# Optimization experiments

Measured on AMD Instinct MI355X. Metric: run time of the kernel, lower is better.

Reference implementation:

```python
import jax, jax.numpy as jnp
import numpy as np

B, N, C, HEADS = 4, 8192, 512, 8


def setup_inputs() -> dict:
    key = jax.random.key(0)
    k1, k2, k3, k4, k5 = jax.random.split(key, 5)
    s = 1.0 / np.sqrt(C)
    return {
        "x": jax.random.normal(k1, (B, N, C), dtype=jnp.float32),
        "w_qkv": jax.random.normal(k2, (3 * C, C), dtype=jnp.float32) * s,
        "b_qkv": jax.random.normal(k3, (3 * C,), dtype=jnp.float32) * 0.01,
        "w_fc": jax.random.normal(k4, (C, C), dtype=jnp.float32) * s,
        "b_fc": jax.random.normal(k5, (C,), dtype=jnp.float32) * 0.01,
        "heads": HEADS,
    }


def reference(x, w_qkv, b_qkv, w_fc, b_fc, heads):
    b, n, c = x.shape
    d = c // heads
    scale = d ** (-0.5)
    # torch Linear: y = x @ W.T + b
    qkv = (x @ w_qkv.T + b_qkv).reshape(b, n, 3, heads, d)
    q, k, v = qkv[:, :, 0], qkv[:, :, 1], qkv[:, :, 2]  # [b,n,h,d]
    # NOTE: source does NOT move heads to dim 1, so attention is over the
    # heads axis: dots is [b, n, h, h].
    dots = jnp.einsum("bnhd,bngd->bnhg", q, k) * scale
    dots = jnp.clip(dots, -50.0, 50.0)
    attn = jax.nn.softmax(dots, axis=-1)
    out = jnp.einsum("bnhg,bngd->bnhd", attn, v)  # [b,n,h,d]
    # transpose(1,2).reshape(B,N,C) exactly as in torch (scrambles n/h)
    out = out.transpose(0, 2, 1, 3).reshape(b, n, c)
    return out @ w_fc.T + b_fc
```

## Files before the change

### kernel.cpp

```cpp
#include <hip/hip_runtime.h>
#include <hip/hip_bf16.h>
#include <stdint.h>


typedef __bf16 bf16x8 __attribute__((ext_vector_type(8)));
typedef float f32x4 __attribute__((ext_vector_type(4)));

__device__ __forceinline__ unsigned short f2bf(float f) {
  unsigned u = __float_as_uint(f);
  u += 0x7fffu + ((u >> 16) & 1u);
  return (unsigned short)(u >> 16);
}
__device__ __forceinline__ unsigned pk2(float a, float b) {
  return (unsigned)f2bf(a) | ((unsigned)f2bf(b) << 16);
}
__device__ __forceinline__ void unpk2(unsigned u, float& a, float& b) {
  a = __uint_as_float(u << 16);
  b = __uint_as_float(u & 0xffff0000u);
}
__device__ __forceinline__ void gload_lds16(const void* g, void* l) {
  __builtin_amdgcn_global_load_lds((const __attribute__((address_space(1))) void*)g,
                                   (__attribute__((address_space(3))) void*)l,
                                   16, 0, 0);
}

__global__ __launch_bounds__(256) void cvt_all(const float* __restrict__ x,
                                               const float* __restrict__ wq,
                                               const float* __restrict__ wf,
                                               unsigned short* __restrict__ xb,
                                               unsigned short* __restrict__ wqb,
                                               unsigned short* __restrict__ wfb) {
  const int n0 = 2097152;
  const int n1 = 98304;
  int i = blockIdx.x * 256 + threadIdx.x;
  const float* in;
  unsigned short* ob;
  int j;
  if (i < n0) {
    in = x; ob = xb; j = i;
  } else if (i < n0 + n1) {
    in = wq; ob = wqb; j = i - n0;
  } else {
    in = wf; ob = wfb; j = i - n0 - n1;
  }
  const float4* p = (const float4*)in;
  float4 a = p[j * 2];
  float4 b = p[j * 2 + 1];
  uint4 o;
  o.x = pk2(a.x, a.y);
  o.y = pk2(a.z, a.w);
  o.z = pk2(b.x, b.y);
  o.w = pk2(b.z, b.w);
  ((uint4*)ob)[j] = o;
}


#define STG(S, BUF)                                                                       \
  do {                                                                                    \
    int _k0 = (S) * 32;                                                                   \
    gload_lds16(Ag + (size_t)(bm0 + srowA0) * KDIM + _k0 + skofA0,                        \
                lds + (BUF) * 24576 + dstA0);                                             \
    gload_lds16(Ag + (size_t)(bm0 + srowA1) * KDIM + _k0 + skofA1,                        \
                lds + (BUF) * 24576 + dstA1);                                             \
    gload_lds16(Bg + (size_t)(bn0 + srowB) * KDIM + _k0 + skofB,                          \
                lds + (BUF) * 24576 + 16384 + dstB);                                      \
  } while (0)

#define STEP(S, BC, BN)                                                                   \
  do {                                                                                    \
    const int s_ = (S);                                                                   \
    asm volatile("s_waitcnt vmcnt(0)" ::: "memory");             \
    __builtin_amdgcn_s_barrier();                                \
    __builtin_amdgcn_sched_barrier(0);                                                    \
    if (s_ + 2 < NKT) STG(s_ + 2, (s_ + 2) % 3);                                          \
    const char* nab = lds + ((s_ + 1) % 3) * 24576 + wm * 4096 + pbase;                   \
    const char* nbb = lds + ((s_ + 1) % 3) * 24576 + 16384 + wn * 4096 + pbase;           \
    if (s_ + 1 < NKT) {                                                                   \
      BN[0] = *(const bf16x8*)(nbb);                                                      \
      BN[1] = *(const bf16x8*)(nbb + 1024);                                               \
      BN[2] = *(const bf16x8*)(nbb + 2048);                                               \
      BN[3] = *(const bf16x8*)(nbb + 3072);                                               \
    }                                                                                     \
    __builtin_amdgcn_s_setprio(1);                                                        \
    _Pragma("unroll") for (int _i = 0; _i < 4; ++_i) {                                    \
      acc[_i][0] = __builtin_amdgcn_mfma_f32_16x16x32_bf16(af[_i], BC[0], acc[_i][0], 0, 0, 0); \
      acc[_i][1] = __builtin_amdgcn_mfma_f32_16x16x32_bf16(af[_i], BC[1], acc[_i][1], 0, 0, 0); \
      acc[_i][2] = __builtin_amdgcn_mfma_f32_16x16x32_bf16(af[_i], BC[2], acc[_i][2], 0, 0, 0); \
      acc[_i][3] = __builtin_amdgcn_mfma_f32_16x16x32_bf16(af[_i], BC[3], acc[_i][3], 0, 0, 0); \
      if (s_ + 1 < NKT) af[_i] = *(const bf16x8*)(nab + _i * 1024);                       \
    }                                                                                     \
    __builtin_amdgcn_s_setprio(0);                                                        \
  } while (0)

template <bool OUT_BF16, int KDIM>
__global__ __launch_bounds__(512, 4) void gemmp(const __hip_bfloat16* __restrict__ Ag,
                                                const __hip_bfloat16* __restrict__ Bg,
                                                const float* __restrict__ bias,
                                                void* __restrict__ C,
                                                int M, int N, int NT) {
  __shared__ __align__(16) char lds[73728];

  const int tid = threadIdx.x;
  const int wv = tid >> 6;
  const int ln = tid & 63;
  const int lrow = ln & 15;
  const int kg = ln >> 4;
  const int wm = wv >> 1;
  const int wn = wv & 1;

  int nwg = gridDim.x;
  int cpx = nwg >> 3;
  int bs = (blockIdx.x & 7) * cpx + (blockIdx.x >> 3);
  const int bm0 = (bs / NT) * 256;
  const int bn0 = (bs % NT) * 128;

  const int pbase = (lrow >> 1) * 128 + ((((lrow & 1) << 2) | kg) ^ ((lrow >> 1) & 7)) * 16;

  int srowA0, skofA0, dstA0, srowA1, skofA1, dstA1, srowB, skofB, dstB;
  {
    int L0 = wv * 1024 + ln * 16;
    int rp0 = L0 >> 7, T0 = ((L0 >> 4) & 7) ^ (rp0 & 7);
    srowA0 = rp0 * 2 + (T0 >> 2);
    skofA0 = (T0 & 3) * 8;
    dstA0 = wv * 1024;
    int L1 = 8192 + L0;
    int rp1 = L1 >> 7, T1 = ((L1 >> 4) & 7) ^ (rp1 & 7);
    srowA1 = rp1 * 2 + (T1 >> 2);
    skofA1 = (T1 & 3) * 8;
    dstA1 = 8192 + wv * 1024;
    srowB = srowA0;
    skofB = skofA0;
    dstB = wv * 1024;
  }

  f32x4 acc[4][4] = {};
  bf16x8 af[4], bs0[4], bs1[4];

  constexpr int NKT = KDIM >> 5;

  STG(0, 0);
  STG(1, 1);
  asm volatile("s_waitcnt vmcnt(3)" ::: "memory");
  __builtin_amdgcn_s_barrier();
  __builtin_amdgcn_sched_barrier(0);
  {
    const char* ab0 = lds + wm * 4096 + pbase;
    const char* bb0 = lds + 16384 + wn * 4096 + pbase;
#pragma unroll
    for (int i = 0; i < 4; ++i) af[i] = *(const bf16x8*)(ab0 + i * 1024);
#pragma unroll
    for (int j = 0; j < 4; ++j) bs0[j] = *(const bf16x8*)(bb0 + j * 1024);
  }

#pragma unroll
  for (int sp = 0; sp < NKT / 2; ++sp) {
    STEP(2 * sp, bs0, bs1);
    STEP(2 * sp + 1, bs1, bs0);
  }
  __syncthreads();

  if (OUT_BF16) {
    unsigned short* tile = (unsigned short*)lds;
#pragma unroll
    for (int fi = 0; fi < 4; ++fi) {
#pragma unroll
      for (int cj = 0; cj < 4; ++cj) {
        int col = wn * 64 + cj * 16 + lrow;
        float bv = bias[bn0 + col];
#pragma unroll
        for (int r = 0; r < 4; ++r) {
          int row = wm * 64 + fi * 16 + kg * 4 + r;
          int sc = (((col >> 3) ^ (row & 7)) << 3) | (col & 7);
          tile[row * 128 + sc] = f2bf(acc[fi][cj][r] + bv);
        }
      }
    }
    __syncthreads();
#pragma unroll
    for (int it = 0; it < 8; ++it) {
      int id = it * 512 + tid;
      int row = id >> 4;
      int c = id & 15;
      uint4 v = *(const uint4*)(lds + row * 256 + ((c ^ (row & 7)) << 4));
      *(uint4*)((unsigned short*)C + (size_t)(bm0 + row) * N + bn0 + c * 8) = v;
    }
  } else {
    float* tilef = (float*)lds;
#pragma unroll
    for (int pass = 0; pass < 2; ++pass) {
      if ((wm >> 1) == pass) {
#pragma unroll
        for (int fi = 0; fi < 4; ++fi) {
#pragma unroll
          for (int cj = 0; cj < 4; ++cj) {
            int col = wn * 64 + cj * 16 + lrow;
            float bv = bias[bn0 + col];
#pragma unroll
            for (int r = 0; r < 4; ++r) {
              int row = (wm & 1) * 64 + fi * 16 + kg * 4 + r;
              int sc = (((col >> 2) ^ (row & 7)) << 2) | (col & 3);
              tilef[row * 128 + sc] = acc[fi][cj][r] + bv;
            }
          }
        }
      }
      __syncthreads();
#pragma unroll
      for (int it = 0; it < 8; ++it) {
        int id = it * 512 + tid;
        int row = id >> 5;
        int c = id & 31;
        uint4 v = *(const uint4*)(lds + row * 512 + ((c ^ (row & 7)) << 4));
        *(uint4*)((float*)C + (size_t)(bm0 + pass * 128 + row) * N + bn0 + c * 4) = v;
      }
      __syncthreads();
    }
  }
}

__global__ __launch_bounds__(256) void attn_tok(const __hip_bfloat16* __restrict__ qkv,
                                                __hip_bfloat16* __restrict__ outp,
                                                int ntok, int npb) {
  const int wv = threadIdx.x >> 6;
  const int ln = threadIdx.x & 63;
  const int t = blockIdx.x * 4 + wv;
  if (t >= ntok) return;
  const int m = ln & 7;

  const __hip_bfloat16* row = qkv + (size_t)t * 1536;
  uint4 qr = *(const uint4*)(row + ln * 8);
  uint4 kr = *(const uint4*)(row + 512 + ln * 8);
  uint4 vr = *(const uint4*)(row + 1024 + ln * 8);

  float qf[8];
  unpk2(qr.x, qf[0], qf[1]);
  unpk2(qr.y, qf[2], qf[3]);
  unpk2(qr.z, qf[4], qf[5]);
  unpk2(qr.w, qf[6], qf[7]);
  unsigned kw[4] = {kr.x, kr.y, kr.z, kr.w};
  unsigned vw[4] = {vr.x, vr.y, vr.z, vr.w};

  float dt[8];
#pragma unroll
  for (int g = 0; g < 8; ++g) {
    int src = g * 8 + m;
    float s = 0.f;
#pragma unroll
    for (int j4 = 0; j4 < 4; ++j4) {
      unsigned kk = __shfl(kw[j4], src, 64);
      float a, b;
      unpk2(kk, a, b);
      s += qf[j4 * 2] * a + qf[j4 * 2 + 1] * b;
    }
    s += __shfl_xor(s, 1, 64);
    s += __shfl_xor(s, 2, 64);
    s += __shfl_xor(s, 4, 64);
    dt[g] = s;
  }

  float mx = -1e30f;
#pragma unroll
  for (int g = 0; g < 8; ++g) {
    dt[g] = fminf(fmaxf(dt[g] * 0.125f, -50.f), 50.f);
    mx = fmaxf(mx, dt[g]);
  }
  float p[8], ssum = 0.f;
#pragma unroll
  for (int g = 0; g < 8; ++g) {
    p[g] = __expf(dt[g] - mx);
    ssum += p[g];
  }
  float inv = 1.f / ssum;

  float o[8] = {0, 0, 0, 0, 0, 0, 0, 0};
#pragma unroll
  for (int g = 0; g < 8; ++g) {
    int src = g * 8 + m;
    float ag = p[g] * inv;
#pragma unroll
    for (int j4 = 0; j4 < 4; ++j4) {
      unsigned vv = __shfl(vw[j4], src, 64);
      float a, b;
      unpk2(vv, a, b);
      o[j4 * 2] += ag * a;
      o[j4 * 2 + 1] += ag * b;
    }
  }

  const int h = ln >> 3;
  const int b = t / npb, n = t % npb;
  size_t dst = (size_t)b * npb * 512 + (size_t)(h * (npb >> 3) + (n >> 3)) * 512 +
               (size_t)((n & 7) * 64 + m * 8);
  uint4 ov;
  ov.x = pk2(o[0], o[1]);
  ov.y = pk2(o[2], o[3]);
  ov.z = pk2(o[4], o[5]);
  ov.w = pk2(o[6], o[7]);
  *(uint4*)(outp + dst) = ov;
}

extern "C" void kernel_launch(void* const* d_in, const int* in_sizes, int n_in,
                              void* d_out, int out_size, void* d_ws, size_t ws_size,
                              hipStream_t stream) {
  const float* x = (const float*)d_in[0];
  const float* w_qkv = (const float*)d_in[1];
  const float* b_qkv = (const float*)d_in[2];
  const float* w_fc = (const float*)d_in[3];
  const float* b_fc = (const float*)d_in[4];
  float* out = (float*)d_out;

  const int M = 32768;
  const int Cc = 512, N3 = 1536;

  __hip_bfloat16* xb = (__hip_bfloat16*)d_ws;
  __hip_bfloat16* wqkvb = xb + (size_t)M * Cc;
  __hip_bfloat16* wfcb = wqkvb + (size_t)N3 * Cc;
  __hip_bfloat16* qkvb = wfcb + (size_t)Cc * Cc;
  __hip_bfloat16* attb = qkvb + (size_t)M * N3;

  cvt_all<<<8704, 256, 0, stream>>>(x, w_qkv, w_fc, (unsigned short*)xb,
                                    (unsigned short*)wqkvb, (unsigned short*)wfcb);

  gemmp<true, 512><<<(M / 256) * (N3 / 128), 512, 0, stream>>>(xb, wqkvb, b_qkv, qkvb, M, N3,
                                                               N3 / 128);
  attn_tok<<<M / 4, 256, 0, stream>>>(qkvb, attb, M, 8192);
  gemmp<false, 512><<<(M / 256) * (Cc / 128), 512, 0, stream>>>(attb, wfcb, b_fc, out, M, Cc,
                                                                Cc / 128);
}
```

Measured before the change: 146.3 us.

## Fuse fp32-to-bf16 conversion of x into the QKV GEMM A-tile loader

```diff
diff --git a/kernel.cpp b/kernel.cpp
--- a/kernel.cpp
+++ b/kernel.cpp
@@ -24,24 +24,19 @@
                                    16, 0, 0);
 }
 
-__global__ __launch_bounds__(256) void cvt_all(const float* __restrict__ x,
-                                               const float* __restrict__ wq,
-                                               const float* __restrict__ wf,
-                                               unsigned short* __restrict__ xb,
-                                               unsigned short* __restrict__ wqb,
-                                               unsigned short* __restrict__ wfb) {
-  const int n0 = 2097152;
+__global__ __launch_bounds__(256) void cvt_w(const float* __restrict__ wq,
+                                             const float* __restrict__ wf,
+                                             unsigned short* __restrict__ wqb,
+                                             unsigned short* __restrict__ wfb) {
   const int n1 = 98304;
   int i = blockIdx.x * 256 + threadIdx.x;
   const float* in;
   unsigned short* ob;
   int j;
-  if (i < n0) {
-    in = x; ob = xb; j = i;
-  } else if (i < n0 + n1) {
-    in = wq; ob = wqb; j = i - n0;
+  if (i < n1) {
+    in = wq; ob = wqb; j = i;
   } else {
-    in = wf; ob = wfb; j = i - n0 - n1;
+    in = wf; ob = wfb; j = i - n1;
   }
   const float4* p = (const float4*)in;
   float4 a = p[j * 2];
@@ -55,24 +50,54 @@
 }
 
 
-#define STG(S, BUF)                                                                       \
+#define STG_A_DMA(S, BUF)                                                                 \
   do {                                                                                    \
     int _k0 = (S) * 32;                                                                   \
-    gload_lds16(Ag + (size_t)(bm0 + srowA0) * KDIM + _k0 + skofA0,                        \
+    gload_lds16(Ab + (size_t)(bm0 + srowA0) * KDIM + _k0 + skofA0,                        \
                 lds + (BUF) * 24576 + dstA0);                                             \
-    gload_lds16(Ag + (size_t)(bm0 + srowA1) * KDIM + _k0 + skofA1,                        \
+    gload_lds16(Ab + (size_t)(bm0 + srowA1) * KDIM + _k0 + skofA1,                        \
                 lds + (BUF) * 24576 + dstA1);                                             \
-    gload_lds16(Bg + (size_t)(bn0 + srowB) * KDIM + _k0 + skofB,                          \
-                lds + (BUF) * 24576 + 16384 + dstB);                                      \
+  } while (0)
+
+#define STG_B(S, BUF)                                                                     \
+  gload_lds16(Bg + (size_t)(bn0 + srowB) * KDIM + (S) * 32 + skofB,                       \
+              lds + (BUF) * 24576 + 16384 + dstB)
+
+#define ISSUE_A(S, RG)                                                                    \
+  do {                                                                                    \
+    int _k0 = (S) * 32;                                                                   \
+    const float* _p0 = Af + (size_t)(bm0 + srowA0) * KDIM + _k0 + skofA0;                 \
+    const float* _p1 = Af + (size_t)(bm0 + srowA1) * KDIM + _k0 + skofA1;                 \
+    RG[0] = *(const float4*)(_p0);                                                        \
+    RG[1] = *(const float4*)(_p0 + 4);                                                    \
+    RG[2] = *(const float4*)(_p1);                                                        \
+    RG[3] = *(const float4*)(_p1 + 4);                                                    \
+  } while (0)
+
+#define WRITE_A(S, RG)                                                                    \
+  do {                                                                                    \
+    uint4 _w0{pk2(RG[0].x, RG[0].y), pk2(RG[0].z, RG[0].w),                               \
+              pk2(RG[1].x, RG[1].y), pk2(RG[1].z, RG[1].w)};                              \
+    uint4 _w1{pk2(RG[2].x, RG[2].y), pk2(RG[2].z, RG[2].w),                               \
+              pk2(RG[3].x, RG[3].y), pk2(RG[3].z, RG[3].w)};                              \
+    *(uint4*)(lds + ((S) % 3) * 24576 + dstA0 + ln * 16) = _w0;                           \
+    *(uint4*)(lds + ((S) % 3) * 24576 + dstA1 + ln * 16) = _w1;                           \
   } while (0)
 
 #define STEP(S, BC, BN)                                                                   \
   do {                                                                                    \
     const int s_ = (S);                                                                   \
-    asm volatile("s_waitcnt vmcnt(0)" ::: "memory");             \
-    __builtin_amdgcn_s_barrier();                                \
+    asm volatile("s_waitcnt vmcnt(0) lgkmcnt(0)" ::: "memory");            \
+    __builtin_amdgcn_s_barrier();                                      \
     __builtin_amdgcn_sched_barrier(0);                                                    \
-    if (s_ + 2 < NKT) STG(s_ + 2, (s_ + 2) % 3);                                          \
+    if (s_ + 2 < NKT) {                                                                   \
+      if constexpr (AF32) {                                                               \
+        ISSUE_A(s_ + 2, rgl);                                                             \
+      } else {                                                                            \
+        STG_A_DMA(s_ + 2, (s_ + 2) % 3);                                                  \
+      }                                                                                   \
+      STG_B(s_ + 2, (s_ + 2) % 3);                                                        \
+    }                                                                                     \
     const char* nab = lds + ((s_ + 1) % 3) * 24576 + wm * 4096 + pbase;                   \
     const char* nbb = lds + ((s_ + 1) % 3) * 24576 + 16384 + wn * 4096 + pbase;           \
     if (s_ + 1 < NKT) {                                                                   \
@@ -90,15 +115,21 @@
       if (s_ + 1 < NKT) af[_i] = *(const bf16x8*)(nab + _i * 1024);                       \
     }                                                                                     \
     __builtin_amdgcn_s_setprio(0);                                                        \
+    if constexpr (AF32) {                                                                 \
+      if (s_ + 2 < NKT) WRITE_A(s_ + 2, rgl);            \
+    }                                                                                     \
   } while (0)
 
-template <bool OUT_BF16, int KDIM>
-__global__ __launch_bounds__(512, 4) void gemmp(const __hip_bfloat16* __restrict__ Ag,
+template <bool OUT_BF16, int KDIM, bool AF32>
+__global__ __launch_bounds__(512, 4) void gemmp(const void* __restrict__ Ag_,
                                                 const __hip_bfloat16* __restrict__ Bg,
                                                 const float* __restrict__ bias,
                                                 void* __restrict__ C,
                                                 int M, int N, int NT) {
   __shared__ __align__(16) char lds[73728];
+
+  const float* Af = (const float*)Ag_;
+  const __hip_bfloat16* Ab = (const __hip_bfloat16*)Ag_;
 
   const int tid = threadIdx.x;
   const int wv = tid >> 6;
@@ -135,12 +166,25 @@
 
   f32x4 acc[4][4] = {};
   bf16x8 af[4], bs0[4], bs1[4];
+  float4 rgl[4], rp[4];
 
   constexpr int NKT = KDIM >> 5;
 
-  STG(0, 0);
-  STG(1, 1);
-  asm volatile("s_waitcnt vmcnt(3)" ::: "memory");
+  if constexpr (AF32) {
+    ISSUE_A(0, rgl);
+    STG_B(0, 0);
+    ISSUE_A(1, rp);
+    STG_B(1, 1);
+    WRITE_A(0, rgl);
+    WRITE_A(1, rp);
+    asm volatile("s_waitcnt vmcnt(0) lgkmcnt(0)" ::: "memory");
+  } else {
+    STG_A_DMA(0, 0);
+    STG_B(0, 0);
+    STG_A_DMA(1, 1);
+    STG_B(1, 1);
+    asm volatile("s_waitcnt vmcnt(3)" ::: "memory");
+  }
   __builtin_amdgcn_s_barrier();
   __builtin_amdgcn_sched_barrier(0);
   {
@@ -312,18 +356,16 @@
   const int M = 32768;
   const int Cc = 512, N3 = 1536;
 
-  __hip_bfloat16* xb = (__hip_bfloat16*)d_ws;
-  __hip_bfloat16* wqkvb = xb + (size_t)M * Cc;
+  __hip_bfloat16* wqkvb = (__hip_bfloat16*)d_ws;
   __hip_bfloat16* wfcb = wqkvb + (size_t)N3 * Cc;
   __hip_bfloat16* qkvb = wfcb + (size_t)Cc * Cc;
   __hip_bfloat16* attb = qkvb + (size_t)M * N3;
 
-  cvt_all<<<8704, 256, 0, stream>>>(x, w_qkv, w_fc, (unsigned short*)xb,
-                                    (unsigned short*)wqkvb, (unsigned short*)wfcb);
-
-  gemmp<true, 512><<<(M / 256) * (N3 / 128), 512, 0, stream>>>(xb, wqkvb, b_qkv, qkvb, M, N3,
-                                                               N3 / 128);
+  cvt_w<<<512, 256, 0, stream>>>(w_qkv, w_fc, (unsigned short*)wqkvb, (unsigned short*)wfcb);
+
+  gemmp<true, 512, true><<<(M / 256) * (N3 / 128), 512, 0, stream>>>(
+      x, wqkvb, b_qkv, qkvb, M, N3, N3 / 128);
   attn_tok<<<M / 4, 256, 0, stream>>>(qkvb, attb, M, 8192);
-  gemmp<false, 512><<<(M / 256) * (Cc / 128), 512, 0, stream>>>(attb, wfcb, b_fc, out, M, Cc,
-                                                                Cc / 128);
-}
+  gemmp<false, 512, false><<<(M / 256) * (Cc / 128), 512, 0, stream>>>(
+      attb, wfcb, b_fc, out, M, Cc, Cc / 128);
+}
```

After: 193.0 us. 31.9% more time.

## Load B operand directly from global into registers, bypassing LDS staging

Applied to the files above, without the earlier changes.

```diff
diff --git a/kernel.cpp b/kernel.cpp
--- a/kernel.cpp
+++ b/kernel.cpp
@@ -55,32 +55,32 @@
 }
 
 
-#define STG(S, BUF)                                                                       \
+#define STG_A(S, BUF)                                                                     \
   do {                                                                                    \
     int _k0 = (S) * 32;                                                                   \
     gload_lds16(Ag + (size_t)(bm0 + srowA0) * KDIM + _k0 + skofA0,                        \
-                lds + (BUF) * 24576 + dstA0);                                             \
+                lds + (BUF) * 16384 + dstA0);                                             \
     gload_lds16(Ag + (size_t)(bm0 + srowA1) * KDIM + _k0 + skofA1,                        \
-                lds + (BUF) * 24576 + dstA1);                                             \
-    gload_lds16(Bg + (size_t)(bn0 + srowB) * KDIM + _k0 + skofB,                          \
-                lds + (BUF) * 24576 + 16384 + dstB);                                      \
+                lds + (BUF) * 16384 + dstA1);                                             \
+  } while (0)
+
+#define LOADB(S, RG)                                                                      \
+  do {                                                                                    \
+    RG[0] = *(const bf16x8*)(bbase + (S) * 32);                                           \
+    RG[1] = *(const bf16x8*)(bbase + 16 * KDIM + (S) * 32);                               \
+    RG[2] = *(const bf16x8*)(bbase + 32 * KDIM + (S) * 32);                               \
+    RG[3] = *(const bf16x8*)(bbase + 48 * KDIM + (S) * 32);                               \
   } while (0)
 
 #define STEP(S, BC, BN)                                                                   \
   do {                                                                                    \
     const int s_ = (S);                                                                   \
-    asm volatile("s_waitcnt vmcnt(0)" ::: "memory");             \
+    asm volatile("s_waitcnt vmcnt(0)" ::: "memory");        \
     __builtin_amdgcn_s_barrier();                                \
     __builtin_amdgcn_sched_barrier(0);                                                    \
-    if (s_ + 2 < NKT) STG(s_ + 2, (s_ + 2) % 3);                                          \
-    const char* nab = lds + ((s_ + 1) % 3) * 24576 + wm * 4096 + pbase;                   \
-    const char* nbb = lds + ((s_ + 1) % 3) * 24576 + 16384 + wn * 4096 + pbase;           \
-    if (s_ + 1 < NKT) {                                                                   \
-      BN[0] = *(const bf16x8*)(nbb);                                                      \
-      BN[1] = *(const bf16x8*)(nbb + 1024);                                               \
-      BN[2] = *(const bf16x8*)(nbb + 2048);                                               \
-      BN[3] = *(const bf16x8*)(nbb + 3072);                                               \
-    }                                                                                     \
+    if (s_ + 2 < NKT) STG_A(s_ + 2, (s_ + 2) % 3);                                        \
+    if (s_ + 1 < NKT) LOADB(s_ + 1, BN);                                                  \
+    const char* nab = lds + ((s_ + 1) % 3) * 16384 + wm * 4096 + pbase;                   \
     __builtin_amdgcn_s_setprio(1);                                                        \
     _Pragma("unroll") for (int _i = 0; _i < 4; ++_i) {                                    \
       acc[_i][0] = __builtin_amdgcn_mfma_f32_16x16x32_bf16(af[_i], BC[0], acc[_i][0], 0, 0, 0); \
@@ -98,7 +98,7 @@
                                                 const float* __restrict__ bias,
                                                 void* __restrict__ C,
                                                 int M, int N, int NT) {
-  __shared__ __align__(16) char lds[73728];
+  __shared__ __align__(16) char lds[65536];
 
   const int tid = threadIdx.x;
   const int wv = tid >> 6;
@@ -116,7 +116,7 @@
 
   const int pbase = (lrow >> 1) * 128 + ((((lrow & 1) << 2) | kg) ^ ((lrow >> 1) & 7)) * 16;
 
-  int srowA0, skofA0, dstA0, srowA1, skofA1, dstA1, srowB, skofB, dstB;
+  int srowA0, skofA0, dstA0, srowA1, skofA1, dstA1;
   {
     int L0 = wv * 1024 + ln * 16;
     int rp0 = L0 >> 7, T0 = ((L0 >> 4) & 7) ^ (rp0 & 7);
@@ -128,28 +128,25 @@
     srowA1 = rp1 * 2 + (T1 >> 2);
     skofA1 = (T1 & 3) * 8;
     dstA1 = 8192 + wv * 1024;
-    srowB = srowA0;
-    skofB = skofA0;
-    dstB = wv * 1024;
-  }
+  }
+
+  const __hip_bfloat16* bbase = Bg + (size_t)(bn0 + wn * 64 + lrow) * KDIM + kg * 8;
 
   f32x4 acc[4][4] = {};
   bf16x8 af[4], bs0[4], bs1[4];
 
   constexpr int NKT = KDIM >> 5;
 
-  STG(0, 0);
-  STG(1, 1);
-  asm volatile("s_waitcnt vmcnt(3)" ::: "memory");
+  STG_A(0, 0);
+  LOADB(0, bs0);
+  STG_A(1, 1);
+  asm volatile("s_waitcnt vmcnt(2)" ::: "memory");
   __builtin_amdgcn_s_barrier();
   __builtin_amdgcn_sched_barrier(0);
   {
     const char* ab0 = lds + wm * 4096 + pbase;
-    const char* bb0 = lds + 16384 + wn * 4096 + pbase;
 #pragma unroll
     for (int i = 0; i < 4; ++i) af[i] = *(const bf16x8*)(ab0 + i * 1024);
-#pragma unroll
-    for (int j = 0; j < 4; ++j) bs0[j] = *(const bf16x8*)(bb0 + j * 1024);
   }
 
 #pragma unroll
```

After: 224.4 us. 1.53x slower.

## Use dedicated smaller-tile double-buffered GEMM for output projection

Applied to the files above, without the earlier changes.

```diff
diff --git a/kernel.cpp b/kernel.cpp
--- a/kernel.cpp
+++ b/kernel.cpp
@@ -54,7 +54,6 @@
   ((uint4*)ob)[j] = o;
 }
 
-
 #define STG(S, BUF)                                                                       \
   do {                                                                                    \
     int _k0 = (S) * 32;                                                                   \
@@ -69,8 +68,8 @@
 #define STEP(S, BC, BN)                                                                   \
   do {                                                                                    \
     const int s_ = (S);                                                                   \
-    asm volatile("s_waitcnt vmcnt(0)" ::: "memory");             \
-    __builtin_amdgcn_s_barrier();                                \
+    asm volatile("s_waitcnt vmcnt(0)" ::: "memory");                                      \
+    __builtin_amdgcn_s_barrier();                                                         \
     __builtin_amdgcn_sched_barrier(0);                                                    \
     if (s_ + 2 < NKT) STG(s_ + 2, (s_ + 2) % 3);                                          \
     const char* nab = lds + ((s_ + 1) % 3) * 24576 + wm * 4096 + pbase;                   \
@@ -92,12 +91,12 @@
     __builtin_amdgcn_s_setprio(0);                                                        \
   } while (0)
 
-template <bool OUT_BF16, int KDIM>
-__global__ __launch_bounds__(512, 4) void gemmp(const __hip_bfloat16* __restrict__ Ag,
-                                                const __hip_bfloat16* __restrict__ Bg,
-                                                const float* __restrict__ bias,
-                                                void* __restrict__ C,
-                                                int M, int N, int NT) {
+template <int KDIM>
+__global__ __launch_bounds__(512, 4) void gemm_qkv(const __hip_bfloat16* __restrict__ Ag,
+                                                   const __hip_bfloat16* __restrict__ Bg,
+                                                   const float* __restrict__ bias,
+                                                   void* __restrict__ C,
+                                                   int M, int N, int NT) {
   __shared__ __align__(16) char lds[73728];
 
   const int tid = threadIdx.x;
@@ -159,62 +158,166 @@
   }
   __syncthreads();
 
-  if (OUT_BF16) {
-    unsigned short* tile = (unsigned short*)lds;
-#pragma unroll
-    for (int fi = 0; fi < 4; ++fi) {
-#pragma unroll
-      for (int cj = 0; cj < 4; ++cj) {
-        int col = wn * 64 + cj * 16 + lrow;
-        float bv = bias[bn0 + col];
-#pragma unroll
-        for (int r = 0; r < 4; ++r) {
-          int row = wm * 64 + fi * 16 + kg * 4 + r;
-          int sc = (((col >> 3) ^ (row & 7)) << 3) | (col & 7);
-          tile[row * 128 + sc] = f2bf(acc[fi][cj][r] + bv);
-        }
+  unsigned short* tile = (unsigned short*)lds;
+#pragma unroll
+  for (int fi = 0; fi < 4; ++fi) {
+#pragma unroll
+    for (int cj = 0; cj < 4; ++cj) {
+      int col = wn * 64 + cj * 16 + lrow;
+      float bv = bias[bn0 + col];
+#pragma unroll
+      for (int r = 0; r < 4; ++r) {
+        int row = wm * 64 + fi * 16 + kg * 4 + r;
+        int sc = (((col >> 3) ^ (row & 7)) << 3) | (col & 7);
+        tile[row * 128 + sc] = f2bf(acc[fi][cj][r] + bv);
       }
     }
-    __syncthreads();
-#pragma unroll
-    for (int it = 0; it < 8; ++it) {
-      int id = it * 512 + tid;
-      int row = id >> 4;
-      int c = id & 15;
-      uint4 v = *(const uint4*)(lds + row * 256 + ((c ^ (row & 7)) << 4));
-      *(uint4*)((unsigned short*)C + (size_t)(bm0 + row) * N + bn0 + c * 8) = v;
-    }
-  } else {
-    float* tilef = (float*)lds;
-#pragma unroll
-    for (int pass = 0; pass < 2; ++pass) {
-      if ((wm >> 1) == pass) {
-#pragma unroll
-        for (int fi = 0; fi < 4; ++fi) {
-#pragma unroll
-          for (int cj = 0; cj < 4; ++cj) {
-            int col = wn * 64 + cj * 16 + lrow;
-            float bv = bias[bn0 + col];
-#pragma unroll
-            for (int r = 0; r < 4; ++r) {
-              int row = (wm & 1) * 64 + fi * 16 + kg * 4 + r;
-              int sc = (((col >> 2) ^ (row & 7)) << 2) | (col & 3);
-              tilef[row * 128 + sc] = acc[fi][cj][r] + bv;
-            }
+  }
+  __syncthreads();
+#pragma unroll
+  for (int it = 0; it < 8; ++it) {
+    int id = it * 512 + tid;
+    int row = id >> 4;
+    int c = id & 15;
+    uint4 v = *(const uint4*)(lds + row * 256 + ((c ^ (row & 7)) << 4));
+    *(uint4*)((unsigned short*)C + (size_t)(bm0 + row) * N + bn0 + c * 8) = v;
+  }
+}
+
+#define FSTG(S, BUF)                                                                      \
+  do {                                                                                    \
+    int _k0 = (S) * 32;                                                                   \
+    gload_lds16(Ag + (size_t)(bm0 + srowA0) * KDIM + _k0 + skofA0,                        \
+                lds + (BUF) * 16384 + dstA0);                                             \
+    gload_lds16(Ag + (size_t)(bm0 + srowA1) * KDIM + _k0 + skofA1,                        \
+                lds + (BUF) * 16384 + dstA1);                                             \
+    gload_lds16(Bg + (size_t)(bn0 + srowB0) * KDIM + _k0 + skofB0,                        \
+                lds + (BUF) * 16384 + 8192 + dstB0);                                      \
+    gload_lds16(Bg + (size_t)(bn0 + srowB1) * KDIM + _k0 + skofB1,                        \
+                lds + (BUF) * 16384 + 8192 + dstB1);                                      \
+  } while (0)
+
+template <int KDIM>
+__global__ __launch_bounds__(256, 4) void gemm_fc(const __hip_bfloat16* __restrict__ Ag,
+                                                  const __hip_bfloat16* __restrict__ Bg,
+                                                  const float* __restrict__ bias,
+                                                  float* __restrict__ C,
+                                                  int M, int N, int NT) {
+  __shared__ __align__(16) char lds[32768];
+
+  const int tid = threadIdx.x;
+  const int wv = tid >> 6;
+  const int ln = tid & 63;
+  const int lrow = ln & 15;
+  const int kg = ln >> 4;
+  const int wm = wv >> 1;
+  const int wn = wv & 1;
+
+  int nwg = gridDim.x;
+  int cpx = nwg >> 3;
+  int bs = (blockIdx.x & 7) * cpx + (blockIdx.x >> 3);
+  const int bm0 = (bs / NT) * 128;
+  const int bn0 = (bs % NT) * 128;
+
+  const int pbase = (lrow >> 1) * 128 + ((((lrow & 1) << 2) | kg) ^ ((lrow >> 1) & 7)) * 16;
+
+  int srowA0, skofA0, dstA0, srowA1, skofA1, dstA1;
+  int srowB0, skofB0, dstB0, srowB1, skofB1, dstB1;
+  {
+    int L0 = wv * 1024 + ln * 16;
+    int rp0 = L0 >> 7, T0 = ((L0 >> 4) & 7) ^ (rp0 & 7);
+    srowA0 = rp0 * 2 + (T0 >> 2);
+    skofA0 = (T0 & 3) * 8;
+    dstA0 = wv * 1024;
+    int L1 = 4096 + L0;
+    int rp1 = L1 >> 7, T1 = ((L1 >> 4) & 7) ^ (rp1 & 7);
+    srowA1 = rp1 * 2 + (T1 >> 2);
+    skofA1 = (T1 & 3) * 8;
+    dstA1 = 4096 + wv * 1024;
+    srowB0 = srowA0; skofB0 = skofA0; dstB0 = dstA0;
+    srowB1 = srowA1; skofB1 = skofA1; dstB1 = dstA1;
+  }
+
+  f32x4 acc[4][4] = {};
+
+  constexpr int NKT = KDIM >> 5;
+
+  FSTG(0, 0);
+  asm volatile("s_waitcnt vmcnt(0)" ::: "memory");
+  __builtin_amdgcn_s_barrier();
+  __builtin_amdgcn_sched_barrier(0);
+
+#pragma unroll
+  for (int s = 0; s < NKT; ++s) {
+    int b = s & 1;
+    if (s + 1 < NKT) FSTG(s + 1, b ^ 1);
+    {
+      const char* ab = lds + b * 16384 + wm * 4096 + pbase;
+      const char* bb = lds + b * 16384 + 8192 + wn * 4096 + pbase;
+      bf16x8 a0 = *(const bf16x8*)(ab);
+      bf16x8 a1 = *(const bf16x8*)(ab + 1024);
+      bf16x8 a2 = *(const bf16x8*)(ab + 2048);
+      bf16x8 a3 = *(const bf16x8*)(ab + 3072);
+      bf16x8 b0 = *(const bf16x8*)(bb);
+      bf16x8 b1 = *(const bf16x8*)(bb + 1024);
+      bf16x8 b2 = *(const bf16x8*)(bb + 2048);
+      bf16x8 b3 = *(const bf16x8*)(bb + 3072);
+      asm volatile("s_waitcnt lgkmcnt(0)" ::: "memory");
+      __builtin_amdgcn_sched_barrier(0);
+      __builtin_amdgcn_s_setprio(1);
+      acc[0][0] = __builtin_amdgcn_mfma_f32_16x16x32_bf16(a0, b0, acc[0][0], 0, 0, 0);
+      acc[0][1] = __builtin_amdgcn_mfma_f32_16x16x32_bf16(a0, b1, acc[0][1], 0, 0, 0);
+      acc[0][2] = __builtin_amdgcn_mfma_f32_16x16x32_bf16(a0, b2, acc[0][2], 0, 0, 0);
+      acc[0][3] = __builtin_amdgcn_mfma_f32_16x16x32_bf16(a0, b3, acc[0][3], 0, 0, 0);
+      acc[1][0] = __builtin_amdgcn_mfma_f32_16x16x32_bf16(a1, b0, acc[1][0], 0, 0, 0);
+      acc[1][1] = __builtin_amdgcn_mfma_f32_16x16x32_bf16(a1, b1, acc[1][1], 0, 0, 0);
+      acc[1][2] = __builtin_amdgcn_mfma_f32_16x16x32_bf16(a1, b2, acc[1][2], 0, 0, 0);
+      acc[1][3] = __builtin_amdgcn_mfma_f32_16x16x32_bf16(a1, b3, acc[1][3], 0, 0, 0);
+      acc[2][0] = __builtin_amdgcn_mfma_f32_16x16x32_bf16(a2, b0, acc[2][0], 0, 0, 0);
+      acc[2][1] = __builtin_amdgcn_mfma_f32_16x16x32_bf16(a2, b1, acc[2][1], 0, 0, 0);
+      acc[2][2] = __builtin_amdgcn_mfma_f32_16x16x32_bf16(a2, b2, acc[2][2], 0, 0, 0);
+      acc[2][3] = __builtin_amdgcn_mfma_f32_16x16x32_bf16(a2, b3, acc[2][3], 0, 0, 0);
+      acc[3][0] = __builtin_amdgcn_mfma_f32_16x16x32_bf16(a3, b0, acc[3][0], 0, 0, 0);
+      acc[3][1] = __builtin_amdgcn_mfma_f32_16x16x32_bf16(a3, b1, acc[3][1], 0, 0, 0);
+      acc[3][2] = __builtin_amdgcn_mfma_f32_16x16x32_bf16(a3, b2, acc[3][2], 0, 0, 0);
+      acc[3][3] = __builtin_amdgcn_mfma_f32_16x16x32_bf16(a3, b3, acc[3][3], 0, 0, 0);
+      __builtin_amdgcn_s_setprio(0);
+    }
+    asm volatile("s_waitcnt vmcnt(0)" ::: "memory");
+    __builtin_amdgcn_s_barrier();
+    __builtin_amdgcn_sched_barrier(0);
+  }
+  __syncthreads();
+
+  float* tilef = (float*)lds;
+#pragma unroll
+  for (int pass = 0; pass < 2; ++pass) {
+    if (wm == pass) {
+#pragma unroll
+      for (int fi = 0; fi < 4; ++fi) {
+#pragma unroll
+        for (int cj = 0; cj < 4; ++cj) {
+          int col = wn * 64 + cj * 16 + lrow;
+          float bv = bias[bn0 + col];
+#pragma unroll
+          for (int r = 0; r < 4; ++r) {
+            int row = fi * 16 + kg * 4 + r;
+            int sc = (((col >> 2) ^ (row & 7)) << 2) | (col & 3);
+            tilef[row * 128 + sc] = acc[fi][cj][r] + bv;
           }
         }
       }
-      __syncthreads();
-#pragma unroll
-      for (int it = 0; it < 8; ++it) {
-        int id = it * 512 + tid;
-        int row = id >> 5;
-        int c = id & 31;
-        uint4 v = *(const uint4*)(lds + row * 512 + ((c ^ (row & 7)) << 4));
-        *(uint4*)((float*)C + (size_t)(bm0 + pass * 128 + row) * N + bn0 + c * 4) = v;
-      }
-      __syncthreads();
-    }
+    }
+    __syncthreads();
+#pragma unroll
+    for (int it = 0; it < 8; ++it) {
+      int id = it * 256 + tid;
+      int row = id >> 5;
+      int c = id & 31;
+      uint4 v = *(const uint4*)(lds + row * 512 + ((c ^ (row & 7)) << 4));
+      *(uint4*)(C + (size_t)(bm0 + pass * 64 + row) * N + bn0 + c * 4) = v;
+    }
+    __syncthreads();
   }
 }
 
@@ -321,9 +424,9 @@
   cvt_all<<<8704, 256, 0, stream>>>(x, w_qkv, w_fc, (unsigned short*)xb,
                                     (unsigned short*)wqkvb, (unsigned short*)wfcb);
 
-  gemmp<true, 512><<<(M / 256) * (N3 / 128), 512, 0, stream>>>(xb, wqkvb, b_qkv, qkvb, M, N3,
-                                                               N3 / 128);
+  gemm_qkv<512><<<(M / 256) * (N3 / 128), 512, 0, stream>>>(xb, wqkvb, b_qkv, qkvb, M, N3,
+                                                            N3 / 128);
   attn_tok<<<M / 4, 256, 0, stream>>>(qkvb, attb, M, 8192);
-  gemmp<false, 512><<<(M / 256) * (Cc / 128), 512, 0, stream>>>(attb, wfcb, b_fc, out, M, Cc,
-                                                                Cc / 128);
-}
+  gemm_fc<512><<<(M / 128) * (Cc / 128), 256, 0, stream>>>(attb, wfcb, b_fc, out, M, Cc,
+                                                           Cc / 128);
+}
```

Result: slower. 150.4 us (+2.8%).
